# Kernel tuning notes

Hardware: AMD Instinct MI355X
Metric: run time of the kernel (lower is better)

The kernel has to match this reference:

```python
import jax, jax.numpy as jnp
import numpy as np

D = 2048      # d_model
QH = 32       # query heads
KVH = 8       # kv heads
HD = D // QH  # head_dim = 64
B = 2
S = 2048
THETA = 1000000.0


def _rope_cos_sin(seq_len, hd, dtype):
    inv_freq = 1.0 / (THETA ** (jnp.arange(0, hd, 2, dtype=jnp.float32) / hd))
    t = jnp.arange(seq_len, dtype=jnp.float32)
    freqs = jnp.einsum('i,j->ij', t, inv_freq)          # [S, hd/2]
    emb = jnp.concatenate([freqs, freqs], axis=-1)      # [S, hd]
    cos = jnp.cos(emb)[None, :, None, :].astype(dtype)  # [1,S,1,hd]
    sin = jnp.sin(emb)[None, :, None, :].astype(dtype)
    return cos, sin


def _rotate_half(x):
    half = x.shape[-1] // 2
    x1, x2 = x[..., :half], x[..., half:]
    return jnp.concatenate([-x2, x1], axis=-1)


def setup_inputs() -> dict:
    key = jax.random.key(0)
    ks = jax.random.split(key, 9)
    inp = {
        'q': jax.random.normal(ks[0], (B, S, D), dtype=jnp.float32),
        'k': jax.random.normal(ks[1], (B, S, D), dtype=jnp.float32),
        'v': jax.random.normal(ks[2], (B, S, D), dtype=jnp.float32),
        'attn_mask': jnp.ones((B, S), dtype=jnp.float32),  # ignored by source math
        'Wq': jax.random.normal(ks[3], (D, D), dtype=jnp.float32) * 0.02,
        'Wk': jax.random.normal(ks[4], (D, KVH * HD), dtype=jnp.float32) * 0.02,
        'Wv': jax.random.normal(ks[5], (D, KVH * HD), dtype=jnp.float32) * 0.02,
        'Wo': jax.random.normal(ks[6], (D, D), dtype=jnp.float32) * 0.02,
        'bo': jnp.zeros((D,), dtype=jnp.float32),
    }
    return inp


def reference(q, k, v, attn_mask, Wq, Wk, Wv, Wo, bo):
    b, s, _ = q.shape
    qh = (q @ Wq).reshape(b, s, QH, HD)
    kh = (k @ Wk).reshape(b, s, KVH, HD)
    vh = (v @ Wv).reshape(b, s, KVH, HD)

    cos, sin = _rope_cos_sin(s, HD, qh.dtype)
    qh = qh * cos + _rotate_half(qh) * sin
    kh = kh * cos + _rotate_half(kh) * sin

    g = QH // KVH
    # torch .repeat tiles the head axis: [h0..h7, h0..h7, ...]
    kh = jnp.tile(kh, (1, 1, g, 1))  # [b,s,QH,HD]
    vh = jnp.tile(vh, (1, 1, g, 1))

    qt = qh.transpose(0, 2, 1, 3)  # [b,QH,s,HD]
    kt = kh.transpose(0, 2, 1, 3)
    vt = vh.transpose(0, 2, 1, 3)

    scale = 1.0 / jnp.sqrt(jnp.asarray(HD, dtype=qt.dtype))
    scores = jnp.einsum('bhqd,bhkd->bhqk', qt, kt) * scale
    # source passes attn_mask=None, is_causal=False when a mask is given:
    # full non-causal attention, mask value unused.
    attn = jax.nn.softmax(scores, axis=-1)
    out = jnp.einsum('bhqk,bhkd->bhqd', attn, vt)
    out = out.transpose(0, 2, 1, 3).reshape(b, s, D)
    return out @ Wo + bo
```

## Files before the change

kernel.cpp:

```cpp
#include <hip/hip_runtime.h>
#include <math.h>

#define D_    2048
#define QH_   32
#define KVH_  8
#define HD_   64
#define B_    2
#define S_    2048
#define NROW_ (B_*S_)
#define KVD_  (KVH_*HD_)
#define LOG2E 1.44269504f

typedef __bf16 bf16;
typedef __bf16 bf16x2 __attribute__((ext_vector_type(2)));
typedef __bf16 bf16x4 __attribute__((ext_vector_type(4)));
typedef __bf16 bf16x8 __attribute__((ext_vector_type(8)));
typedef float  f32x4  __attribute__((ext_vector_type(4)));
typedef float  f32x16 __attribute__((ext_vector_type(16)));

__device__ __forceinline__ f32x4 mfma16(bf16x8 a, bf16x8 b, f32x4 c) {
  return __builtin_amdgcn_mfma_f32_16x16x32_bf16(a, b, c, 0, 0, 0);
}
__device__ __forceinline__ f32x16 mfma32(bf16x8 a, bf16x8 b, f32x16 c) {
  return __builtin_amdgcn_mfma_f32_32x32x16_bf16(a, b, c, 0, 0, 0);
}

__device__ __forceinline__ void gload_lds16(const bf16* g, bf16* l) {
  __builtin_amdgcn_global_load_lds(
      (const __attribute__((address_space(1))) void*)g,
      (__attribute__((address_space(3))) void*)l, 16, 0, 0);
}

__device__ __forceinline__ unsigned pack_bf16(float a, float b) {
  union { bf16x2 v; unsigned u; } t;
  t.v[0] = (bf16)a; t.v[1] = (bf16)b;
  return t.u;
}

__global__ void k_ropetab(float2* __restrict__ tab) {
  int idx = blockIdx.x * 256 + threadIdx.x;
  int s = idx >> 5, d = idx & 31;
  float invf = exp2f(-(float)d * 0.62286151f);
  float ang = (float)s * invf;
  float sn, cs;
  sincosf(ang, &sn, &cs);
  tab[idx] = make_float2(cs, sn);
}

__global__ void k_convert(const float* __restrict__ in, bf16* __restrict__ out, int n4) {
  int i = blockIdx.x * 256 + threadIdx.x;
  if (i >= n4) return;
  f32x4 v = ((const f32x4*)in)[i];
  bf16x4 o;
#pragma unroll
  for (int j = 0; j < 4; j++) o[j] = (bf16)v[j];
  ((bf16x4*)out)[i] = o;
}

__global__ void k_convert2(const float* __restrict__ in0, const float* __restrict__ in1,
                           bf16* __restrict__ o0, bf16* __restrict__ o1, int n4) {
  const float* in = blockIdx.z ? in1 : in0;
  bf16* out = blockIdx.z ? o1 : o0;
  int i = blockIdx.x * 256 + threadIdx.x;
  if (i >= n4) return;
  f32x4 v = ((const f32x4*)in)[i];
  bf16x4 o;
#pragma unroll
  for (int j = 0; j < 4; j++) o[j] = (bf16)v[j];
  ((bf16x4*)out)[i] = o;
}

__device__ __forceinline__ void transpose_w_body(const float* W, bf16* Wt, int K, int N) {
  __shared__ float tile[32][33];
  int n0 = blockIdx.x * 32, k0 = blockIdx.y * 32;
  int tx = threadIdx.x, ty = threadIdx.y;
#pragma unroll
  for (int j = 0; j < 4; j++)
    tile[ty + 8*j][tx] = W[(size_t)(k0 + ty + 8*j) * N + n0 + tx];
  __syncthreads();
#pragma unroll
  for (int j = 0; j < 4; j++)
    Wt[(size_t)(n0 + ty + 8*j) * K + k0 + tx] = (bf16)tile[tx][ty + 8*j];
}

__global__ void k_transpose_w(const float* __restrict__ W, bf16* __restrict__ Wt,
                              int K, int N) {
  transpose_w_body(W, Wt, K, N);
}

__global__ void k_transpose_w2(const float* __restrict__ W0, const float* __restrict__ W1,
                               bf16* __restrict__ T0, bf16* __restrict__ T1) {
  transpose_w_body(blockIdx.z ? W1 : W0, blockIdx.z ? T1 : T0, D_, KVD_);
}

template<int EPI>
__device__ __forceinline__ void gemm_body(const bf16* A, const bf16* Bt, void* Cout,
                                          const float* bias, const float2* tab,
                                          int M, int N, int K) {
  __shared__ alignas(16) bf16 As[2][128 * 64];
  __shared__ alignas(16) bf16 Bs[2][128 * 64];
  int tid = threadIdx.x;
  int wave = tid >> 6, lane = tid & 63, hi = lane >> 4, lr = lane & 15;
  int wm = wave >> 1, wn = wave & 1;
  int m0 = blockIdx.y * 128, n0 = blockIdx.x * 128;
  f32x4 acc[4][4] = {};
  int nk = K >> 6;

  int s_row[4], s_dch[4];
#pragma unroll
  for (int i = 0; i < 4; i++) {
    int c = i * 256 + tid;
    s_row[i] = c >> 3;
    s_dch[i] = (c & 7) ^ (s_row[i] & 7);
  }

#define GSTAGE(buf, kt_)                                                       \
  do {                                                                         \
    int k0_ = (kt_) * 64;                                                      \
    _Pragma("unroll")                                                          \
    for (int i = 0; i < 4; i++) {                                              \
      gload_lds16(A  + (size_t)(m0 + s_row[i]) * K + k0_ + s_dch[i] * 8,       \
                  &As[buf][(i * 256 + (wave * 64)) * 8]);                      \
      gload_lds16(Bt + (size_t)(n0 + s_row[i]) * K + k0_ + s_dch[i] * 8,       \
                  &Bs[buf][(i * 256 + (wave * 64)) * 8]);                      \
    }                                                                          \
  } while (0)

  GSTAGE(0, 0);
  __syncthreads();

  for (int kt = 0; kt < nk; kt++) {
    int cur = kt & 1;
    if (kt + 1 < nk) GSTAGE(cur ^ 1, kt + 1);
#pragma unroll
    for (int kk = 0; kk < 2; kk++) {
      bf16x8 af[4], bfr[4];
#pragma unroll
      for (int mt = 0; mt < 4; mt++) {
        int row = wm * 64 + mt * 16 + lr;
        int sl = (kk * 4 + hi) ^ (row & 7);
        af[mt] = *(const bf16x8*)(&As[cur][row * 64 + sl * 8]);
      }
#pragma unroll
      for (int nt = 0; nt < 4; nt++) {
        int row = wn * 64 + nt * 16 + lr;
        int sl = (kk * 4 + hi) ^ (row & 7);
        bfr[nt] = *(const bf16x8*)(&Bs[cur][row * 64 + sl * 8]);
      }
      __builtin_amdgcn_s_setprio(1);
#pragma unroll
      for (int mt = 0; mt < 4; mt++)
#pragma unroll
        for (int nt = 0; nt < 4; nt++) {
          if (EPI == 3) acc[mt][nt] = mfma16(bfr[nt], af[mt], acc[mt][nt]);
          else          acc[mt][nt] = mfma16(af[mt], bfr[nt], acc[mt][nt]);
        }
      __builtin_amdgcn_s_setprio(0);
    }
    __syncthreads();
  }
#undef GSTAGE

  if (EPI == 3) {
    int b = m0 >> 11;
#pragma unroll
    for (int mt = 0; mt < 4; mt++)
#pragma unroll
      for (int nt = 0; nt < 4; nt++)
#pragma unroll
        for (int r = 0; r < 4; r++) {
          int n = n0 + wn * 64 + nt * 16 + 4 * hi + r;
          int m = m0 + wm * 64 + mt * 16 + lr;
          ((bf16*)Cout)[((size_t)(b * KVD_ + n)) * S_ + (m & (S_ - 1))] =
              (bf16)acc[mt][nt][r];
        }
  } else if (EPI == 1) {
#pragma unroll
    for (int mt = 0; mt < 4; mt++)
#pragma unroll
      for (int r = 0; r < 4; r++) {
        int grow = m0 + wm * 64 + mt * 16 + 4 * hi + r;
        int s = grow & (S_ - 1);
#pragma unroll
        for (int nt = 0; nt < 2; nt++) {
          int gcol = n0 + wn * 64 + nt * 16 + lr;
          float2 cs = tab[s * 32 + nt * 16 + lr];
          float x1 = acc[mt][nt][r], x2 = acc[mt][nt + 2][r];
          ((bf16*)Cout)[(size_t)grow * N + gcol]      = (bf16)(x1 * cs.x - x2 * cs.y);
          ((bf16*)Cout)[(size_t)grow * N + gcol + 32] = (bf16)(x2 * cs.x + x1 * cs.y);
        }
      }
  } else {
#pragma unroll
    for (int mt = 0; mt < 4; mt++)
#pragma unroll
      for (int nt = 0; nt < 4; nt++)
#pragma unroll
        for (int r = 0; r < 4; r++) {
          int grow = m0 + wm * 64 + mt * 16 + 4 * hi + r;
          int gcol = n0 + wn * 64 + nt * 16 + lr;
          ((float*)Cout)[(size_t)grow * N + gcol] = acc[mt][nt][r] + bias[gcol];
        }
  }
}

__global__ __launch_bounds__(256) void k_gemm_q(const bf16* __restrict__ A,
                                                const bf16* __restrict__ Bt,
                                                bf16* __restrict__ C,
                                                const float2* __restrict__ tab) {
  gemm_body<1>(A, Bt, C, nullptr, tab, NROW_, D_, D_);
}

__global__ __launch_bounds__(256) void k_gemm_kv(const bf16* __restrict__ A0,
                                                 const bf16* __restrict__ A1,
                                                 const bf16* __restrict__ B0,
                                                 const bf16* __restrict__ B1,
                                                 bf16* __restrict__ Kh,
                                                 bf16* __restrict__ Vt,
                                                 const float2* __restrict__ tab) {
  if (blockIdx.z == 0) gemm_body<1>(A0, B0, Kh, nullptr, tab, NROW_, KVD_, D_);
  else                 gemm_body<3>(A1, B1, Vt, nullptr, nullptr, NROW_, KVD_, D_);
}

__global__ __launch_bounds__(256) void k_gemm_o(const bf16* __restrict__ A,
                                                const bf16* __restrict__ Bt,
                                                float* __restrict__ C,
                                                const float* __restrict__ bias) {
  gemm_body<2>(A, Bt, C, bias, nullptr, NROW_, D_, D_);
}

__global__ __launch_bounds__(512, 4) void k_attn(const bf16* __restrict__ Qh,
                                                 const bf16* __restrict__ Kh,
                                                 const bf16* __restrict__ Vt,
                                                 bf16* __restrict__ ctx) {
  __shared__ alignas(16) bf16 Ks[2][64 * 64];
  __shared__ alignas(16) bf16 Vs[2][64 * 64];
  int tid = threadIdx.x;
  int wave = tid >> 6, lane = tid & 63, hi2 = lane >> 5, l31 = lane & 31;
  int qt = blockIdx.x, h = blockIdx.y, b = blockIdx.z;
  int kv = h & 7;
  int q0 = qt * 256 + wave * 32;

  bf16x8 qf[4];
  {
    const float QSC = 0.125f * LOG2E;
    const bf16* qp = Qh + (size_t)(b * S_ + q0 + l31) * D_ + h * HD_ + hi2 * 8;
#pragma unroll
    for (int df = 0; df < 4; df++) {
      bf16x8 v = *(const bf16x8*)(qp + 16 * df);
#pragma unroll
      for (int j = 0; j < 8; j++) v[j] = (bf16)((float)v[j] * QSC);
      qf[df] = v;
    }
  }

  f32x16 o0, o1, accl;
#pragma unroll
  for (int i = 0; i < 16; i++) { o0[i] = 0.f; o1[i] = 0.f; accl[i] = 0.f; }
  bf16x8 ones;
#pragma unroll
  for (int j = 0; j < 8; j++) ones[j] = (bf16)1.0f;

  const bf16* Kg = Kh + (size_t)(b * S_) * KVD_ + kv * HD_;
  const bf16* Vg = Vt + (size_t)(b * KVH_ + kv) * HD_ * S_;

  int c_row = tid >> 3, c_slot = tid & 7;
  int c_dch = c_slot ^ (c_row & 7);

#define STAGE(buf, kt_)                                                        \
  do {                                                                         \
    gload_lds16(Kg + (size_t)((kt_) * 64 + c_row) * KVD_ + c_dch * 8,          \
                &Ks[buf][tid * 8]);                                            \
    gload_lds16(Vg + (size_t)c_row * S_ + (kt_) * 64 + c_dch * 8,              \
                &Vs[buf][tid * 8]);                                            \
  } while (0)

  STAGE(0, 0);
  __syncthreads();

  const int NT = S_ / 64;
  for (int kt = 0; kt < NT; kt++) {
    int cur = kt & 1;
    if (kt + 1 < NT) STAGE(cur ^ 1, kt + 1);

    const bf16* Kb = &Ks[cur][0];
    const bf16* Vb = &Vs[cur][0];

    f32x16 s0, s1;
#pragma unroll
    for (int i = 0; i < 16; i++) { s0[i] = 0.f; s1[i] = 0.f; }
    __builtin_amdgcn_s_setprio(1);
#pragma unroll
    for (int df = 0; df < 4; df++) {
      int ch = hi2 + 2 * df;
      int sl = (ch ^ (l31 & 7)) << 3;
      bf16x8 k0 = *(const bf16x8*)(Kb + l31 * 64 + sl);
      bf16x8 k1 = *(const bf16x8*)(Kb + (l31 + 32) * 64 + sl);
      s0 = mfma32(k0, qf[df], s0);
      s1 = mfma32(k1, qf[df], s1);
    }
    __builtin_amdgcn_s_setprio(0);

#pragma unroll
    for (int i = 0; i < 16; i++) s0[i] = __builtin_amdgcn_exp2f(s0[i]);
#pragma unroll
    for (int i = 0; i < 16; i++) s1[i] = __builtin_amdgcn_exp2f(s1[i]);

    unsigned Rk[2][4][2];
#pragma unroll
    for (int m = 0; m < 4; m++)
#pragma unroll
      for (int w = 0; w < 2; w++) {
        Rk[0][m][w] = pack_bf16(s0[4*m + 2*w], s0[4*m + 2*w + 1]);
        Rk[1][m][w] = pack_bf16(s1[4*m + 2*w], s1[4*m + 2*w + 1]);
      }
#pragma unroll
    for (int kf = 0; kf < 2; kf++)
#pragma unroll
      for (int kp = 0; kp < 2; kp++)
#pragma unroll
        for (int w = 0; w < 2; w++)
          asm volatile("v_permlane32_swap_b32 %0, %1"
                       : "+v"(Rk[kf][2*kp][w]), "+v"(Rk[kf][2*kp+1][w]));
    bf16x8 pf[4];
#pragma unroll
    for (int kfr = 0; kfr < 4; kfr++) {
      int kf = kfr >> 1, k2 = (kfr & 1) * 2;
      union { unsigned d[4]; bf16x8 v; } u;
      u.d[0] = Rk[kf][k2][0];     u.d[1] = Rk[kf][k2][1];
      u.d[2] = Rk[kf][k2 + 1][0]; u.d[3] = Rk[kf][k2 + 1][1];
      pf[kfr] = u.v;
    }

    __builtin_amdgcn_s_setprio(1);
#pragma unroll
    for (int kfr = 0; kfr < 4; kfr++) {
      int ch = hi2 + 2 * kfr;
      int sl = (ch ^ (l31 & 7)) << 3;
      bf16x8 v0 = *(const bf16x8*)(Vb + l31 * 64 + sl);
      bf16x8 v1 = *(const bf16x8*)(Vb + (l31 + 32) * 64 + sl);
      o0 = mfma32(pf[kfr], v0, o0);
      o1 = mfma32(pf[kfr], v1, o1);
      accl = mfma32(pf[kfr], ones, accl);
    }
    __builtin_amdgcn_s_setprio(0);
    __syncthreads();
  }
#undef STAGE

#pragma unroll
  for (int r = 0; r < 16; r++) {
    int rowq = (r & 3) + 8 * (r >> 2) + 4 * hi2;
    float inv = 1.f / accl[r];
    size_t base = (size_t)(b * S_ + q0 + rowq) * D_ + h * HD_;
    ctx[base + l31]      = (bf16)(o0[r] * inv);
    ctx[base + l31 + 32] = (bf16)(o1[r] * inv);
  }
}

extern "C" void kernel_launch(void* const* d_in, const int* in_sizes, int n_in,
                              void* d_out, int out_size, void* d_ws, size_t ws_size,
                              hipStream_t stream) {
  const float* q  = (const float*)d_in[0];
  const float* k  = (const float*)d_in[1];
  const float* v  = (const float*)d_in[2];
  const float* Wq = (const float*)d_in[4];
  const float* Wk = (const float*)d_in[5];
  const float* Wv = (const float*)d_in[6];
  const float* Wo = (const float*)d_in[7];
  const float* bo = (const float*)d_in[8];

  char* ws = (char*)d_ws;
  bf16*   A0  = (bf16*)(ws + 0);
  bf16*   A1  = (bf16*)(ws + 16777216);
  bf16*   Wt  = (bf16*)(ws + 33554432);
  bf16*   Qh  = (bf16*)(ws + 41943040);
  bf16*   Kh  = (bf16*)(ws + 58720256);
  bf16*   Vt  = (bf16*)(ws + 62914560);
  float2* tab = (float2*)(ws + 67108864);
  bf16*   WtK = Wt;
  bf16*   WtV = (bf16*)(ws + 33554432 + 2097152);
  bf16*   ctx = A1;

  const int n4 = NROW_ * D_ / 4;

  k_ropetab<<<(S_ * 32) / 256, 256, 0, stream>>>(tab);
  k_convert<<<n4 / 256, 256, 0, stream>>>(q, A0, n4);
  k_transpose_w<<<dim3(D_/32, D_/32), dim3(32, 8), 0, stream>>>(Wq, Wt, D_, D_);
  k_gemm_q<<<dim3(D_/128, NROW_/128), 256, 0, stream>>>(A0, Wt, Qh, tab);
  k_convert2<<<dim3(n4 / 256, 1, 2), 256, 0, stream>>>(k, v, A0, A1, n4);
  k_transpose_w2<<<dim3(KVD_/32, D_/32, 2), dim3(32, 8), 0, stream>>>(Wk, Wv, WtK, WtV);
  k_gemm_kv<<<dim3(KVD_/128, NROW_/128, 2), 256, 0, stream>>>(A0, A1, WtK, WtV, Kh, Vt, tab);
  k_attn<<<dim3(S_/256, QH_, B_), 512, 0, stream>>>(Qh, Kh, Vt, ctx);
  k_transpose_w<<<dim3(D_/32, D_/32), dim3(32, 8), 0, stream>>>(Wo, Wt, D_, D_);
  k_gemm_o<<<dim3(D_/128, NROW_/128), 256, 0, stream>>>(ctx, Wt, (float*)d_out, bo);
}
```

Before: 259.2 us.

## Process two query tiles per wave in attention and compute row sums on VALU

The attention kernel now runs 4 waves per block, each handling 64 query rows as two 32-row tiles. Each K/V fragment read from LDS feeds MFMAs for both tiles, and the staging loop is split into two chunks per thread so the shared-memory tile stays the same size. The softmax denominator moves from an extra MFMA against a ones vector to a VALU sum of the exponentials, combined across lanes with shuffles at the end. This removes a third of the PV-stage MFMAs and halves LDS traffic per MFMA, at the cost of more accumulator registers and possibly lower occupancy.

```diff
diff --git a/kernel.cpp b/kernel.cpp
--- a/kernel.cpp
+++ b/kernel.cpp
@@ -229,7 +229,7 @@
   gemm_body<2>(A, Bt, C, bias, nullptr, NROW_, D_, D_);
 }
 
-__global__ __launch_bounds__(512, 4) void k_attn(const bf16* __restrict__ Qh,
+__global__ __launch_bounds__(256, 2) void k_attn(const bf16* __restrict__ Qh,
                                                  const bf16* __restrict__ Kh,
                                                  const bf16* __restrict__ Vt,
                                                  bf16* __restrict__ ctx) {
@@ -239,40 +239,51 @@
   int wave = tid >> 6, lane = tid & 63, hi2 = lane >> 5, l31 = lane & 31;
   int qt = blockIdx.x, h = blockIdx.y, b = blockIdx.z;
   int kv = h & 7;
-  int q0 = qt * 256 + wave * 32;
-
-  bf16x8 qf[4];
+  int q0 = qt * 256 + wave * 64;
+
+  bf16x8 qfA[4], qfB[4];
   {
     const float QSC = 0.125f * LOG2E;
-    const bf16* qp = Qh + (size_t)(b * S_ + q0 + l31) * D_ + h * HD_ + hi2 * 8;
+    const bf16* qpA = Qh + (size_t)(b * S_ + q0 + l31) * D_ + h * HD_ + hi2 * 8;
+    const bf16* qpB = qpA + (size_t)32 * D_;
 #pragma unroll
     for (int df = 0; df < 4; df++) {
-      bf16x8 v = *(const bf16x8*)(qp + 16 * df);
-#pragma unroll
-      for (int j = 0; j < 8; j++) v[j] = (bf16)((float)v[j] * QSC);
-      qf[df] = v;
-    }
-  }
-
-  f32x16 o0, o1, accl;
-#pragma unroll
-  for (int i = 0; i < 16; i++) { o0[i] = 0.f; o1[i] = 0.f; accl[i] = 0.f; }
-  bf16x8 ones;
-#pragma unroll
-  for (int j = 0; j < 8; j++) ones[j] = (bf16)1.0f;
+      bf16x8 va = *(const bf16x8*)(qpA + 16 * df);
+      bf16x8 vb = *(const bf16x8*)(qpB + 16 * df);
+#pragma unroll
+      for (int j = 0; j < 8; j++) {
+        va[j] = (bf16)((float)va[j] * QSC);
+        vb[j] = (bf16)((float)vb[j] * QSC);
+      }
+      qfA[df] = va; qfB[df] = vb;
+    }
+  }
+
+  float lA = 0.f, lB = 0.f;
+  f32x16 o0A, o1A, o0B, o1B;
+#pragma unroll
+  for (int i = 0; i < 16; i++) { o0A[i] = 0.f; o1A[i] = 0.f; o0B[i] = 0.f; o1B[i] = 0.f; }
 
   const bf16* Kg = Kh + (size_t)(b * S_) * KVD_ + kv * HD_;
   const bf16* Vg = Vt + (size_t)(b * KVH_ + kv) * HD_ * S_;
 
-  int c_row = tid >> 3, c_slot = tid & 7;
-  int c_dch = c_slot ^ (c_row & 7);
+  int c_row[2], c_dch[2];
+#pragma unroll
+  for (int i = 0; i < 2; i++) {
+    int c = i * 256 + tid;
+    c_row[i] = c >> 3;
+    c_dch[i] = (c & 7) ^ (c_row[i] & 7);
+  }
 
 #define STAGE(buf, kt_)                                                        \
   do {                                                                         \
-    gload_lds16(Kg + (size_t)((kt_) * 64 + c_row) * KVD_ + c_dch * 8,          \
-                &Ks[buf][tid * 8]);                                            \
-    gload_lds16(Vg + (size_t)c_row * S_ + (kt_) * 64 + c_dch * 8,              \
-                &Vs[buf][tid * 8]);                                            \
+    _Pragma("unroll")                                                          \
+    for (int i = 0; i < 2; i++) {                                              \
+      gload_lds16(Kg + (size_t)((kt_) * 64 + c_row[i]) * KVD_ + c_dch[i] * 8,  \
+                  &Ks[buf][(i * 256 + tid) * 8]);                              \
+      gload_lds16(Vg + (size_t)c_row[i] * S_ + (kt_) * 64 + c_dch[i] * 8,      \
+                  &Vs[buf][(i * 256 + tid) * 8]);                              \
+    }                                                                          \
   } while (0)
 
   STAGE(0, 0);
@@ -286,9 +297,9 @@
     const bf16* Kb = &Ks[cur][0];
     const bf16* Vb = &Vs[cur][0];
 
-    f32x16 s0, s1;
-#pragma unroll
-    for (int i = 0; i < 16; i++) { s0[i] = 0.f; s1[i] = 0.f; }
+    f32x16 s0A, s1A, s0B, s1B;
+#pragma unroll
+    for (int i = 0; i < 16; i++) { s0A[i] = 0.f; s1A[i] = 0.f; s0B[i] = 0.f; s1B[i] = 0.f; }
     __builtin_amdgcn_s_setprio(1);
 #pragma unroll
     for (int df = 0; df < 4; df++) {
@@ -296,40 +307,52 @@
       int sl = (ch ^ (l31 & 7)) << 3;
       bf16x8 k0 = *(const bf16x8*)(Kb + l31 * 64 + sl);
       bf16x8 k1 = *(const bf16x8*)(Kb + (l31 + 32) * 64 + sl);
-      s0 = mfma32(k0, qf[df], s0);
-      s1 = mfma32(k1, qf[df], s1);
+      s0A = mfma32(k0, qfA[df], s0A);
+      s1A = mfma32(k1, qfA[df], s1A);
+      s0B = mfma32(k0, qfB[df], s0B);
+      s1B = mfma32(k1, qfB[df], s1B);
     }
     __builtin_amdgcn_s_setprio(0);
 
-#pragma unroll
-    for (int i = 0; i < 16; i++) s0[i] = __builtin_amdgcn_exp2f(s0[i]);
-#pragma unroll
-    for (int i = 0; i < 16; i++) s1[i] = __builtin_amdgcn_exp2f(s1[i]);
-
-    unsigned Rk[2][4][2];
-#pragma unroll
-    for (int m = 0; m < 4; m++)
-#pragma unroll
-      for (int w = 0; w < 2; w++) {
-        Rk[0][m][w] = pack_bf16(s0[4*m + 2*w], s0[4*m + 2*w + 1]);
-        Rk[1][m][w] = pack_bf16(s1[4*m + 2*w], s1[4*m + 2*w + 1]);
+    float rsA = 0.f, rsB = 0.f;
+#pragma unroll
+    for (int i = 0; i < 16; i++) {
+      s0A[i] = __builtin_amdgcn_exp2f(s0A[i]); rsA += s0A[i];
+      s1A[i] = __builtin_amdgcn_exp2f(s1A[i]); rsA += s1A[i];
+      s0B[i] = __builtin_amdgcn_exp2f(s0B[i]); rsB += s0B[i];
+      s1B[i] = __builtin_amdgcn_exp2f(s1B[i]); rsB += s1B[i];
+    }
+    lA += rsA; lB += rsB;
+
+    bf16x8 pfA[4], pfB[4];
+#pragma unroll
+    for (int g = 0; g < 2; g++) {
+      f32x16& t0 = g ? s0B : s0A;
+      f32x16& t1 = g ? s1B : s1A;
+      unsigned Rk[2][4][2];
+#pragma unroll
+      for (int m = 0; m < 4; m++)
+#pragma unroll
+        for (int w = 0; w < 2; w++) {
+          Rk[0][m][w] = pack_bf16(t0[4*m + 2*w], t0[4*m + 2*w + 1]);
+          Rk[1][m][w] = pack_bf16(t1[4*m + 2*w], t1[4*m + 2*w + 1]);
+        }
+#pragma unroll
+      for (int kf = 0; kf < 2; kf++)
+#pragma unroll
+        for (int kp = 0; kp < 2; kp++)
+#pragma unroll
+          for (int w = 0; w < 2; w++)
+            asm volatile("v_permlane32_swap_b32 %0, %1"
+                         : "+v"(Rk[kf][2*kp][w]), "+v"(Rk[kf][2*kp+1][w]));
+#pragma unroll
+      for (int kfr = 0; kfr < 4; kfr++) {
+        int kf = kfr >> 1, k2 = (kfr & 1) * 2;
+        union { unsigned d[4]; bf16x8 v; } u;
+        u.d[0] = Rk[kf][k2][0];     u.d[1] = Rk[kf][k2][1];
+        u.d[2] = Rk[kf][k2 + 1][0]; u.d[3] = Rk[kf][k2 + 1][1];
+        if (g) pfB[kfr] = u.v; else pfA[kfr] = u.v;
       }
-#pragma unroll
-    for (int kf = 0; kf < 2; kf++)
-#pragma unroll
-      for (int kp = 0; kp < 2; kp++)
-#pragma unroll
-        for (int w = 0; w < 2; w++)
-          asm volatile("v_permlane32_swap_b32 %0, %1"
-                       : "+v"(Rk[kf][2*kp][w]), "+v"(Rk[kf][2*kp+1][w]));
-    bf16x8 pf[4];
-#pragma unroll
-    for (int kfr = 0; kfr < 4; kfr++) {
-      int kf = kfr >> 1, k2 = (kfr & 1) * 2;
-      union { unsigned d[4]; bf16x8 v; } u;
-      u.d[0] = Rk[kf][k2][0];     u.d[1] = Rk[kf][k2][1];
-      u.d[2] = Rk[kf][k2 + 1][0]; u.d[3] = Rk[kf][k2 + 1][1];
-      pf[kfr] = u.v;
     }
 
     __builtin_amdgcn_s_setprio(1);
@@ -339,22 +362,29 @@
       int sl = (ch ^ (l31 & 7)) << 3;
       bf16x8 v0 = *(const bf16x8*)(Vb + l31 * 64 + sl);
       bf16x8 v1 = *(const bf16x8*)(Vb + (l31 + 32) * 64 + sl);
-      o0 = mfma32(pf[kfr], v0, o0);
-      o1 = mfma32(pf[kfr], v1, o1);
-      accl = mfma32(pf[kfr], ones, accl);
+      o0A = mfma32(pfA[kfr], v0, o0A);
+      o1A = mfma32(pfA[kfr], v1, o1A);
+      o0B = mfma32(pfB[kfr], v0, o0B);
+      o1B = mfma32(pfB[kfr], v1, o1B);
     }
     __builtin_amdgcn_s_setprio(0);
     __syncthreads();
   }
 #undef STAGE
 
+  float lAf = lA + __shfl_xor(lA, 32, 64);
+  float lBf = lB + __shfl_xor(lB, 32, 64);
 #pragma unroll
   for (int r = 0; r < 16; r++) {
     int rowq = (r & 3) + 8 * (r >> 2) + 4 * hi2;
-    float inv = 1.f / accl[r];
-    size_t base = (size_t)(b * S_ + q0 + rowq) * D_ + h * HD_;
-    ctx[base + l31]      = (bf16)(o0[r] * inv);
-    ctx[base + l31 + 32] = (bf16)(o1[r] * inv);
+    float invA = 1.f / __shfl(lAf, rowq, 64);
+    float invB = 1.f / __shfl(lBf, rowq, 64);
+    size_t baseA = (size_t)(b * S_ + q0 + rowq) * D_ + h * HD_;
+    size_t baseB = baseA + (size_t)32 * D_;
+    ctx[baseA + l31]      = (bf16)(o0A[r] * invA);
+    ctx[baseA + l31 + 32] = (bf16)(o1A[r] * invA);
+    ctx[baseB + l31]      = (bf16)(o0B[r] * invB);
+    ctx[baseB + l31 + 32] = (bf16)(o1B[r] * invB);
   }
 }
 
@@ -391,7 +421,7 @@
   k_convert2<<<dim3(n4 / 256, 1, 2), 256, 0, stream>>>(k, v, A0, A1, n4);
   k_transpose_w2<<<dim3(KVD_/32, D_/32, 2), dim3(32, 8), 0, stream>>>(Wk, Wv, WtK, WtV);
   k_gemm_kv<<<dim3(KVD_/128, NROW_/128, 2), 256, 0, stream>>>(A0, A1, WtK, WtV, Kh, Vt, tab);
-  k_attn<<<dim3(S_/256, QH_, B_), 512, 0, stream>>>(Qh, Kh, Vt, ctx);
+  k_attn<<<dim3(S_/256, QH_, B_), 256, 0, stream>>>(Qh, Kh, Vt, ctx);
   k_transpose_w<<<dim3(D_/32, D_/32), dim3(32, 8), 0, stream>>>(Wo, Wt, D_, D_);
   k_gemm_o<<<dim3(D_/128, NROW_/128), 256, 0, stream>>>(ctx, Wt, (float*)d_out, bo);
 }
```

After: 254.7 us. No clear change (-1.7%).
